# Kernel tuning notes

Measured on AMD Instinct MI355X. Metric: run time of the kernel, lower is better.

## Reference

```python
import jax, jax.numpy as jnp
import numpy as np

TEMPERATURE = 0.07
NEG_INF = -9e15
EPS = 1e-8  # matches torch F.cosine_similarity eps default


def setup_inputs() -> dict:
    key = jax.random.key(0)
    k1, k2 = jax.random.split(key)
    N, D = 4096, 512
    z1 = jax.random.normal(k1, (N, D), dtype=jnp.float32)
    z2 = jax.random.normal(k2, (N, D), dtype=jnp.float32)
    return {"z1": z1, "z2": z2}


def reference(z1, z2):
    N = z1.shape[0]
    z = jnp.concatenate([z1, z2], axis=0)  # [2N, D]
    # cosine similarity as normalized GEMM (torch clamps norm by eps)
    norm = jnp.maximum(jnp.linalg.norm(z, axis=-1, keepdims=True), EPS)
    zn = z / norm
    sim = (zn @ zn.T) / TEMPERATURE  # [2N, 2N]
    two_n = 2 * N
    idx = jnp.arange(two_n)
    sim = sim.at[idx, idx].set(NEG_INF)
    # positives: diag(sim, N) then diag(sim, -N)
    pos_upper = sim[idx[:N], idx[:N] + N]
    pos_lower = sim[idx[:N] + N, idx[:N]]
    positives = jnp.concatenate([pos_upper, pos_lower], axis=0)  # [2N]
    loss = -positives + jax.scipy.special.logsumexp(sim, axis=1)
    return loss.mean()
```

## Files before the change

kernel.cpp:

```cpp
#include <hip/hip_runtime.h>
#include <hip/hip_bf16.h>
#include <hip/hip_fp8.h>

#define N_ROWS 4096
#define TWO_N 8192
#define DIM 512
#define BKB 64
#define NKS (DIM / BKB)
#define INV_T 14.285714285714286f
#define LOG2E 1.4426950408889634f
#define C_LOG2E 20.60992915555662f
#define INV_SQRT_T 3.7796447300922722f

typedef float f32x4 __attribute__((ext_vector_type(4)));
typedef long fp8x8;
typedef long fp8x8x2 __attribute__((ext_vector_type(2)));

#define ASYNC_COPY16(gp, lp)                                                     \
  __builtin_amdgcn_global_load_lds((const __attribute__((address_space(1))) void*)(gp), \
                                   (__attribute__((address_space(3))) void*)(lp), 16, 0, 0)

#define VMCNT(n) asm volatile("s_waitcnt vmcnt(" #n ")" ::: "memory")

__global__ __launch_bounds__(256) void k_prep(const float* __restrict__ z1,
                                              const float* __restrict__ z2,
                                              unsigned char* __restrict__ zn,
                                              float* __restrict__ posbuf,
                                              float* __restrict__ rowsum) {
  const int t = threadIdx.x;
  const int wv = t >> 6, lane = t & 63;
  const int r = blockIdx.x * 4 + wv;
  if (blockIdx.x < 32) rowsum[blockIdx.x * 256 + t] = 0.f;

  const float4* p1 = reinterpret_cast<const float4*>(z1 + (size_t)r * DIM) + (lane << 1);
  const float4* p2 = reinterpret_cast<const float4*>(z2 + (size_t)r * DIM) + (lane << 1);
  float4 a0 = p1[0], a1 = p1[1];
  float4 b0 = p2[0], b1 = p2[1];

  float s1 = a0.x * a0.x + a0.y * a0.y + a0.z * a0.z + a0.w * a0.w
           + a1.x * a1.x + a1.y * a1.y + a1.z * a1.z + a1.w * a1.w;
  float s2 = b0.x * b0.x + b0.y * b0.y + b0.z * b0.z + b0.w * b0.w
           + b1.x * b1.x + b1.y * b1.y + b1.z * b1.z + b1.w * b1.w;
  float sd = a0.x * b0.x + a0.y * b0.y + a0.z * b0.z + a0.w * b0.w
           + a1.x * b1.x + a1.y * b1.y + a1.z * b1.z + a1.w * b1.w;
#pragma unroll
  for (int off = 1; off < 64; off <<= 1) {
    s1 += __shfl_xor(s1, off, 64);
    s2 += __shfl_xor(s2, off, 64);
    sd += __shfl_xor(sd, off, 64);
  }
  const float sc1 = INV_SQRT_T / fmaxf(sqrtf(s1), 1e-8f);
  const float sc2 = INV_SQRT_T / fmaxf(sqrtf(s2), 1e-8f);

  float va[8] = {a0.x, a0.y, a0.z, a0.w, a1.x, a1.y, a1.z, a1.w};
  float vb[8] = {b0.x, b0.y, b0.z, b0.w, b1.x, b1.y, b1.z, b1.w};
  unsigned long long pa = 0, pb = 0;
#pragma unroll
  for (int d = 0; d < 8; d++) {
    __hip_fp8_e4m3 qa(va[d] * sc1);
    __hip_fp8_e4m3 qb(vb[d] * sc2);
    pa |= (unsigned long long)qa.__x << (8 * d);
    pb |= (unsigned long long)qb.__x << (8 * d);
  }
  const int pofs = (lane >> 3) * 64 + (lane & 3) * 16 + ((lane >> 2) & 1) * 8;
  *reinterpret_cast<unsigned long long*>(zn + (size_t)r * DIM + pofs) = pa;
  *reinterpret_cast<unsigned long long*>(zn + (size_t)(r + N_ROWS) * DIM + pofs) = pb;

  if (lane == 0) posbuf[r] = sd * sc1 * sc2;
}

__global__ __launch_bounds__(256, 3) void k_lse(const unsigned char* __restrict__ Zn,
                                                float* __restrict__ rowsum) {
  __shared__ char smem[49152] __attribute__((aligned(16)));
  const int tid  = threadIdx.x;
  const int wave = tid >> 6;
  const int lane = tid & 63;
  const int cl   = lane & 15;
  const int q    = lane >> 4;

  const int b = (blockIdx.x & 7) * 260 + (blockIdx.x >> 3);

  int rt = (int)((129.0f - sqrtf(16641.0f - 8.0f * (float)b)) * 0.5f);
  if (rt > 63) rt = 63;
  if (rt < 0) rt = 0;
  while (rt > 0 && 64 * rt - rt * (rt - 1) / 2 > b) rt--;
  while (64 * (rt + 1) - (rt + 1) * rt / 2 <= b) rt++;
  const int ct = rt + (b - (64 * rt - rt * (rt - 1) / 2));

  const int wr = (wave >> 1) * 64;
  const int wc = (wave & 1) * 64;

  const int r0  = tid >> 2;
  const int sg  = ((tid & 3) ^ ((r0 >> 1) & 3)) * 16;
  const unsigned char* gA0 = Zn + (size_t)(rt * 128 + r0) * DIM + sg;
  const unsigned char* gB0 = Zn + (size_t)(ct * 128 + r0) * DIM + sg;

  f32x4 acc[4][4] = {};
  const int xk2 = (cl >> 1) & 3;
  const int gofs = ((q ^ xk2) << 4);

#define STAGE(d, it)                                                        \
  {                                                                         \
    char* _b = smem + (d) * 16384 + wave * 1024;                            \
    const int _ko = (it) * BKB;                                             \
    ASYNC_COPY16(gA0 + _ko,            _b);                                 \
    ASYNC_COPY16(gA0 + _ko + 64 * DIM, _b + 4096);                          \
    ASYNC_COPY16(gB0 + _ko,            _b + 8192);                          \
    ASYNC_COPY16(gB0 + _ko + 64 * DIM, _b + 12288);                         \
  }

  STAGE(0, 0);
  STAGE(1, 1);
#pragma unroll
  for (int ks = 0; ks < NKS; ks++) {
    const int cur = ks % 3;
    if (ks + 1 < NKS) { VMCNT(4); } else { VMCNT(0); }
    __builtin_amdgcn_s_barrier();
    asm volatile("" ::: "memory");
    if (ks + 2 < NKS) STAGE((ks + 2) % 3, ks + 2);

    const char* sA = smem + cur * 16384;
    const char* sB = sA + 8192;
    fp8x8 af[2][4], bfr[2][4];
#pragma unroll
    for (int i = 0; i < 4; i++) {
      fp8x8x2 av = *reinterpret_cast<const fp8x8x2*>(sA + (wr + i * 16 + cl) * 64 + gofs);
      af[0][i] = av[0];
      af[1][i] = av[1];
    }
#pragma unroll
    for (int j = 0; j < 4; j++) {
      fp8x8x2 bv = *reinterpret_cast<const fp8x8x2*>(sB + (wc + j * 16 + cl) * 64 + gofs);
      bfr[0][j] = bv[0];
      bfr[1][j] = bv[1];
    }
#pragma unroll
    for (int ksub = 0; ksub < 2; ksub++)
#pragma unroll
      for (int i = 0; i < 4; i++)
#pragma unroll
        for (int j = 0; j < 4; j++)
          acc[i][j] = __builtin_amdgcn_mfma_f32_16x16x32_fp8_fp8(af[ksub][i], bfr[ksub][j],
                                                                 acc[i][j], 0, 0, 0);
  }
#undef STAGE

  const bool diagw = (rt == ct) && (wr == wc);
  float psum[4][4];
#pragma unroll
  for (int i = 0; i < 4; i++)
#pragma unroll
    for (int r = 0; r < 4; r++) psum[i][r] = 0.f;
  float colp[4] = {0.f, 0.f, 0.f, 0.f};

#pragma unroll
  for (int i = 0; i < 4; i++)
#pragma unroll
    for (int j = 0; j < 4; j++)
#pragma unroll
      for (int r = 0; r < 4; r++) {
        float e = exp2f(fmaf(acc[i][j][r], LOG2E, -C_LOG2E));
        if (diagw && (i == j) && (cl == q * 4 + r)) e = 0.f;
        psum[i][r] += e;
        colp[j] += e;
      }

#pragma unroll
  for (int i = 0; i < 4; i++)
#pragma unroll
    for (int r = 0; r < 4; r++) {
      float v = psum[i][r];
      v += __shfl_xor(v, 1, 64);
      v += __shfl_xor(v, 2, 64);
      v += __shfl_xor(v, 4, 64);
      v += __shfl_xor(v, 8, 64);
      if (cl == 0) atomicAdd(&rowsum[rt * 128 + wr + i * 16 + q * 4 + r], v);
    }

  if (rt != ct) {
#pragma unroll
    for (int j = 0; j < 4; j++) {
      float v = colp[j];
      v += __shfl_xor(v, 16, 64);
      v += __shfl_xor(v, 32, 64);
      if (q == 0) atomicAdd(&rowsum[ct * 128 + wc + j * 16 + cl], v);
    }
  }
}

__global__ void k_final(const float* __restrict__ rowsum, const float* __restrict__ posbuf,
                        float* __restrict__ out) {
  __shared__ float red[16];
  const int t = threadIdx.x;
  float s = 0.f;
#pragma unroll
  for (int it = 0; it < TWO_N / 1024; it++) {
    const int row = it * 1024 + t;
    float v = logf(rowsum[row]);
    if (row < N_ROWS) v -= 2.f * posbuf[row];
    s += v;
  }
#pragma unroll
  for (int off = 32; off > 0; off >>= 1) s += __shfl_down(s, off, 64);
  if ((t & 63) == 0) red[t >> 6] = s;
  __syncthreads();
  if (t == 0) {
    float tot = 0.f;
#pragma unroll
    for (int i = 0; i < 16; i++) tot += red[i];
    out[0] = tot / (float)TWO_N + INV_T;
  }
}

extern "C" void kernel_launch(void* const* d_in, const int* in_sizes, int n_in,
                              void* d_out, int out_size, void* d_ws, size_t ws_size,
                              hipStream_t stream) {
  const float* z1 = (const float*)d_in[0];
  const float* z2 = (const float*)d_in[1];
  float* out = (float*)d_out;
  char* ws = (char*)d_ws;

  unsigned char* zn = (unsigned char*)ws;
  float* rowsum = (float*)(ws + 4194304);
  float* posbuf = (float*)(ws + 4227072);

  k_prep<<<1024, 256, 0, stream>>>(z1, z2, zn, posbuf, rowsum);
  k_lse<<<2080, 256, 0, stream>>>(zn, rowsum);
  k_final<<<1, 1024, 0, stream>>>(rowsum, posbuf, out);
}
```

Before: 117.9 us.

## Give each wave private double-buffered LDS tiles to drop block barriers

Each wave now loads its own 64-row A and B slices into a private 16KB LDS region with double buffering, so the per-k-step block-wide s_barrier is removed. The next stage is issued only after that wave's LDS reads finish (lgkmcnt wait plus sched_barrier). The cost is duplicated global/LDS traffic, since A and B tiles are now fetched by two waves each, and 64KB of LDS per block with launch bounds lowered from 3 to 2 blocks per CU, which reduces occupancy.

```diff
diff --git a/kernel.cpp b/kernel.cpp
--- a/kernel.cpp
+++ b/kernel.cpp
@@ -20,7 +20,8 @@
   __builtin_amdgcn_global_load_lds((const __attribute__((address_space(1))) void*)(gp), \
                                    (__attribute__((address_space(3))) void*)(lp), 16, 0, 0)
 
-#define VMCNT(n) asm volatile("s_waitcnt vmcnt(" #n ")" ::: "memory")
+#define VMCNT(n)  asm volatile("s_waitcnt vmcnt(" #n ")" ::: "memory")
+#define LGKM0()   asm volatile("s_waitcnt lgkmcnt(0)" ::: "memory")
 
 __global__ __launch_bounds__(256) void k_prep(const float* __restrict__ z1,
                                               const float* __restrict__ z2,
@@ -69,9 +70,9 @@
   if (lane == 0) posbuf[r] = sd * sc1 * sc2;
 }
 
-__global__ __launch_bounds__(256, 3) void k_lse(const unsigned char* __restrict__ Zn,
+__global__ __launch_bounds__(256, 2) void k_lse(const unsigned char* __restrict__ Zn,
                                                 float* __restrict__ rowsum) {
-  __shared__ char smem[49152] __attribute__((aligned(16)));
+  __shared__ char smem[65536] __attribute__((aligned(16)));
   const int tid  = threadIdx.x;
   const int wave = tid >> 6;
   const int lane = tid & 63;
@@ -90,50 +91,55 @@
   const int wr = (wave >> 1) * 64;
   const int wc = (wave & 1) * 64;
 
-  const int r0  = tid >> 2;
-  const int sg  = ((tid & 3) ^ ((r0 >> 1) & 3)) * 16;
-  const unsigned char* gA0 = Zn + (size_t)(rt * 128 + r0) * DIM + sg;
-  const unsigned char* gB0 = Zn + (size_t)(ct * 128 + r0) * DIM + sg;
+  const int srow = lane >> 2;
+  const int sgr  = ((lane & 3) ^ ((lane >> 3) & 3)) * 16;
+  const unsigned char* gA0 = Zn + (size_t)(rt * 128 + wr + srow) * DIM + sgr;
+  const unsigned char* gB0 = Zn + (size_t)(ct * 128 + wc + srow) * DIM + sgr;
+
+  char* wbase = smem + wave * 16384;
 
   f32x4 acc[4][4] = {};
-  const int xk2 = (cl >> 1) & 3;
-  const int gofs = ((q ^ xk2) << 4);
-
-#define STAGE(d, it)                                                        \
+  const int gofs = ((q ^ ((cl >> 1) & 3)) << 4);
+
+#define STAGE(bufi, it)                                                     \
   {                                                                         \
-    char* _b = smem + (d) * 16384 + wave * 1024;                            \
+    char* _a = wbase + (bufi) * 8192;                                       \
     const int _ko = (it) * BKB;                                             \
-    ASYNC_COPY16(gA0 + _ko,            _b);                                 \
-    ASYNC_COPY16(gA0 + _ko + 64 * DIM, _b + 4096);                          \
-    ASYNC_COPY16(gB0 + _ko,            _b + 8192);                          \
-    ASYNC_COPY16(gB0 + _ko + 64 * DIM, _b + 12288);                         \
+    ASYNC_COPY16(gA0 + _ko,                 _a);                            \
+    ASYNC_COPY16(gA0 + _ko + 16 * DIM,      _a + 1024);                     \
+    ASYNC_COPY16(gA0 + _ko + 32 * DIM,      _a + 2048);                     \
+    ASYNC_COPY16(gA0 + _ko + 48 * DIM,      _a + 3072);                     \
+    ASYNC_COPY16(gB0 + _ko,                 _a + 4096);                     \
+    ASYNC_COPY16(gB0 + _ko + 16 * DIM,      _a + 5120);                     \
+    ASYNC_COPY16(gB0 + _ko + 32 * DIM,      _a + 6144);                     \
+    ASYNC_COPY16(gB0 + _ko + 48 * DIM,      _a + 7168);                     \
   }
 
   STAGE(0, 0);
   STAGE(1, 1);
 #pragma unroll
   for (int ks = 0; ks < NKS; ks++) {
-    const int cur = ks % 3;
-    if (ks + 1 < NKS) { VMCNT(4); } else { VMCNT(0); }
-    __builtin_amdgcn_s_barrier();
-    asm volatile("" ::: "memory");
-    if (ks + 2 < NKS) STAGE((ks + 2) % 3, ks + 2);
-
-    const char* sA = smem + cur * 16384;
-    const char* sB = sA + 8192;
+    if (ks + 1 < NKS) { VMCNT(8); } else { VMCNT(0); }
+
+    const char* sA = wbase + (ks & 1) * 8192;
+    const char* sB = sA + 4096;
     fp8x8 af[2][4], bfr[2][4];
 #pragma unroll
     for (int i = 0; i < 4; i++) {
-      fp8x8x2 av = *reinterpret_cast<const fp8x8x2*>(sA + (wr + i * 16 + cl) * 64 + gofs);
+      fp8x8x2 av = *reinterpret_cast<const fp8x8x2*>(sA + (i * 16 + cl) * 64 + gofs);
       af[0][i] = av[0];
       af[1][i] = av[1];
     }
 #pragma unroll
     for (int j = 0; j < 4; j++) {
-      fp8x8x2 bv = *reinterpret_cast<const fp8x8x2*>(sB + (wc + j * 16 + cl) * 64 + gofs);
+      fp8x8x2 bv = *reinterpret_cast<const fp8x8x2*>(sB + (j * 16 + cl) * 64 + gofs);
       bfr[0][j] = bv[0];
       bfr[1][j] = bv[1];
     }
+    LGKM0();
+    __builtin_amdgcn_sched_barrier(0);
+    if (ks + 2 < NKS) STAGE(ks & 1, ks + 2);
+
 #pragma unroll
     for (int ksub = 0; ksub < 2; ksub++)
 #pragma unroll
```

Result: slower. 128.4 us (+8.9%).
